# Kernel optimization log

Hardware: AMD Instinct MI355X
Metric: run time of the kernel (lower is better)

Reference implementation:

```python
import jax, jax.numpy as jnp
import numpy as np

N_FILTERS = 1024
KH, KW = 5, 5
LOC = 3                      # locality (pad + maxpool kernel/stride)
B, H, W = 1024, 64, 64
WIN = KH + 2 * LOC           # 11: sliced window side after padding


def setup_inputs() -> dict:
    key = jax.random.key(0)
    k1, k2, k3, k4 = jax.random.split(key, 4)
    X = jax.random.normal(k1, (B, 1, H, W), dtype=jnp.float32)
    weight = jax.random.normal(k2, (N_FILTERS, 1, KH, KW), dtype=jnp.float32)
    bias = jax.random.normal(k3, (N_FILTERS,), dtype=jnp.float32)
    # top-left corner (i, j) of each filter's window in the padded image;
    # must satisfy i + KH + 2*LOC <= H + 2*LOC  =>  i in [0, H-KH]
    positions = jax.random.randint(k4, (N_FILTERS, 2), 0, H - KH + 1, dtype=jnp.int32)
    return {"X": X, "weight": weight, "bias": bias, "positions": positions}


def reference(X, weight, bias, positions):
    # ZeroPad2d(locality)
    Xp = jnp.pad(X, ((0, 0), (0, 0), (LOC, LOC), (LOC, LOC)))

    def slice_one(pos):
        return jax.lax.dynamic_slice(Xp, (0, 0, pos[0], pos[1]), (B, 1, WIN, WIN))

    windows = jax.vmap(slice_one)(positions)
    lhs = jnp.transpose(windows[:, :, 0], (1, 0, 2, 3))

    # All n_filters tiny single-channel convs as ONE grouped conv.
    conv = jax.lax.conv_general_dilated(
        lhs, weight, window_strides=(1, 1), padding='VALID',
        dimension_numbers=('NCHW', 'OIHW', 'NCHW'),
        feature_group_count=N_FILTERS)                # [B,F,2L+1,2L+1] = [B,F,7,7]
    conv = conv + bias[None, :, None, None]

    # MaxPool2d((LOC,LOC)) with default stride=LOC, floor mode -> 2x2.
    pooled = jax.lax.reduce_window(
        conv, -jnp.inf, jax.lax.max,
        window_dimensions=(1, 1, LOC, LOC),
        window_strides=(1, 1, LOC, LOC),
        padding='VALID')                              # [B,F,2,2]

    # torch.cat(dim=1) over per-filter [B,1,2,2] tensors + reshape(B,-1)
    return pooled.reshape(B, -1)                      # [B, F*4]
```

## Files before the change

kernel.cpp:

```cpp
#include <hip/hip_runtime.h>

#define N_FILTERS 1024
#define B_TOTAL   1024
#define IMG       64
#define LDS_ROWS  70
#define LDS_STRIDE 76

__global__ void prep_wt_kernel(const float* __restrict__ W, float* __restrict__ Wt) {
    int idx = blockIdx.x * 256 + threadIdx.x;
    if (idx < 25 * N_FILTERS) {
        int k = idx >> 10;
        int f = idx & (N_FILTERS - 1);
        Wt[idx] = W[f * 25 + k];
    }
}

__global__ __launch_bounds__(256, 4) void filters_main(
    const float* __restrict__ X,
    const float* __restrict__ Wg,
    const float* __restrict__ Wt,
    const float* __restrict__ bias,
    const int*   __restrict__ pos,
    float*       __restrict__ out,
    int use_wt)
{
    __shared__ float L[LDS_ROWS * LDS_STRIDE];
    const int b = blockIdx.x;
    const int t = threadIdx.x;

    for (int idx = t; idx < LDS_ROWS * LDS_STRIDE; idx += 256) L[idx] = 0.0f;
    __syncthreads();

    const float4* X4 = (const float4*)(X + (size_t)b * (IMG * IMG));
    for (int q = t; q < (IMG * IMG / 4); q += 256) {
        int r  = q >> 4;
        int c4 = q & 15;
        float4 v = X4[q];
        *(float4*)&L[(r + 3) * LDS_STRIDE + 4 + (c4 << 2)] = v;
    }
    __syncthreads();

    #pragma unroll 1
    for (int chunk = 0; chunk < 4; ++chunk) {
        const int f = t + (chunk << 8);
        const int i = pos[2 * f];
        const int j = pos[2 * f + 1];

        float w[25];
        if (use_wt) {
            #pragma unroll
            for (int k = 0; k < 25; ++k) w[k] = Wt[k * N_FILTERS + f];
        } else {
            #pragma unroll
            for (int k = 0; k < 25; ++k) w[k] = Wg[f * 25 + k];
        }

        float acc[6][6];
        #pragma unroll
        for (int y = 0; y < 6; ++y)
            #pragma unroll
            for (int x = 0; x < 6; ++x) acc[y][x] = 0.0f;

        const float* Lb = &L[i * LDS_STRIDE + j + 1];
        #pragma unroll
        for (int wr = 0; wr < 10; ++wr) {
            float in[10];
            #pragma unroll
            for (int wc = 0; wc < 10; ++wc) in[wc] = Lb[wr * LDS_STRIDE + wc];
            #pragma unroll
            for (int y = 0; y < 6; ++y) {
                if (y >= ((wr > 4) ? (wr - 4) : 0) && y <= ((wr < 5) ? wr : 5)) {
                    const int r = wr - y;
                    #pragma unroll
                    for (int x = 0; x < 6; ++x) {
                        #pragma unroll
                        for (int c = 0; c < 5; ++c)
                            acc[y][x] = fmaf(w[r * 5 + c], in[x + c], acc[y][x]);
                    }
                }
            }
        }

        const float bv = bias[f];
        float p[2][2];
        #pragma unroll
        for (int py = 0; py < 2; ++py) {
            #pragma unroll
            for (int px = 0; px < 2; ++px) {
                float m = acc[3 * py][3 * px];
                #pragma unroll
                for (int dy = 0; dy < 3; ++dy)
                    #pragma unroll
                    for (int dx = 0; dx < 3; ++dx)
                        m = fmaxf(m, acc[3 * py + dy][3 * px + dx]);
                p[py][px] = m + bv;
            }
        }

        float4 o;
        o.x = p[0][0]; o.y = p[0][1]; o.z = p[1][0]; o.w = p[1][1];
        *(float4*)&out[(size_t)b * (N_FILTERS * 4) + (f << 2)] = o;
    }
}

extern "C" void kernel_launch(void* const* d_in, const int* in_sizes, int n_in,
                              void* d_out, int out_size, void* d_ws, size_t ws_size,
                              hipStream_t stream) {
    const float* X    = (const float*)d_in[0];
    const float* W    = (const float*)d_in[1];
    const float* bias = (const float*)d_in[2];
    const int*   pos  = (const int*)d_in[3];
    float* out = (float*)d_out;
    float* Wt  = (float*)d_ws;

    const int use_wt = (ws_size >= (size_t)(25 * N_FILTERS * sizeof(float))) ? 1 : 0;
    if (use_wt) {
        prep_wt_kernel<<<(25 * N_FILTERS + 255) / 256, 256, 0, stream>>>(W, Wt);
    }
    filters_main<<<B_TOTAL, 256, 0, stream>>>(X, W, Wt, bias, pos, out, use_wt);
}
```

Baseline: 107.0 us.

## Recast per-filter local convs as fp16 MFMA GEMMs over batch with Toeplitz weights

The image is converted to fp16 and stored in a batch-interleaved octet layout. Each filter's 5x5 kernel is expanded into a Toeplitz-style A matrix (36 outputs by 240 window taps), so the per-filter conv over the batch runs as 16x16x32 MFMA ops instead of scalar FMAs. Work is redistributed to one block per filter and batch quarter. Max-pooling is done through LDS. Precision drops to fp16 inputs, and the fixed-size workspace is assumed large enough without any check.

```diff
diff --git a/kernel.cpp b/kernel.cpp
--- a/kernel.cpp
+++ b/kernel.cpp
@@ -1,105 +1,163 @@
 #include <hip/hip_runtime.h>
 
-#define N_FILTERS 1024
-#define B_TOTAL   1024
-#define IMG       64
-#define LDS_ROWS  70
-#define LDS_STRIDE 76
 
-__global__ void prep_wt_kernel(const float* __restrict__ W, float* __restrict__ Wt) {
-    int idx = blockIdx.x * 256 + threadIdx.x;
-    if (idx < 25 * N_FILTERS) {
-        int k = idx >> 10;
-        int f = idx & (N_FILTERS - 1);
-        Wt[idx] = W[f * 25 + k];
+#define PAD_DIM   70
+#define OCT_BYTES 16384
+#define XH_BYTES  ((size_t)700 * OCT_BYTES)
+#define WF_FILTER 24576
+
+typedef _Float16 v8h __attribute__((ext_vector_type(8)));
+typedef float    v4f __attribute__((ext_vector_type(4)));
+
+__global__ __launch_bounds__(256) void prep_kernel(
+    const float* __restrict__ X, const float* __restrict__ W,
+    const int* __restrict__ pos,
+    _Float16* __restrict__ Xh, _Float16* __restrict__ Wf)
+{
+    const int bid = blockIdx.x;
+    const int t   = threadIdx.x;
+    if (bid < 1024) {
+        __shared__ float T[64 * 65];
+        const int r = bid >> 4, bgrp = bid & 15;
+        #pragma unroll
+        for (int i = 0; i < 16; ++i) {
+            int flat = i * 256 + t;
+            int b = flat >> 6, c = flat & 63;
+            T[b * 65 + c] = X[(size_t)(bgrp * 64 + b) * 4096 + r * 64 + c];
+        }
+        __syncthreads();
+        for (int idx = t; idx < 9 * 64; idx += 256) {
+            int o = idx >> 6, b = idx & 63;
+            v8h v;
+            #pragma unroll
+            for (int e = 0; e < 8; ++e) {
+                int c = 8 * o + e - 3;
+                v[e] = (c >= 0 && c < 64) ? (_Float16)T[b * 65 + c] : (_Float16)0.f;
+            }
+            *(v8h*)((char*)Xh + (size_t)((r + 3) * 10 + o) * OCT_BYTES
+                              + (bgrp * 64 + b) * 16) = v;
+        }
+    } else if (bid < 1148) {
+        int zi = bid - 1024, oct;
+        if (zi < 60) { int pr = zi / 10; pr = pr < 3 ? pr : pr + 64; oct = pr * 10 + zi % 10; }
+        else         { oct = (3 + (zi - 60)) * 10 + 9; }
+        uint4* q = (uint4*)((char*)Xh + (size_t)oct * OCT_BYTES);
+        uint4 z = {0, 0, 0, 0};
+        for (int i = t; i < 1024; i += 256) q[i] = z;
+    } else {
+        const int f = bid - 1148;
+        __shared__ _Float16 wl[25];
+        if (t < 25) wl[t] = (_Float16)W[f * 25 + t];
+        const int sjoff = pos[2 * f + 1] & 7;
+        __syncthreads();
+        for (int flat = t; flat < 1536; flat += 256) {
+            int s  = flat / 192;
+            int r1 = flat - s * 192;
+            int mt = r1 >> 6, ln = r1 & 63;
+            int m    = mt * 16 + (ln & 15);
+            int kb   = s * 32 + (ln >> 4) * 8;
+            v8h v;
+            if (m < 36 && kb < 240) {
+                int y  = (m * 43) >> 8;
+                int x  = m - 6 * y;
+                int wr = (kb * 171) >> 12;
+                int r_ = wr - y;
+                int rem0 = kb - wr * 24;
+                #pragma unroll
+                for (int e = 0; e < 8; ++e) {
+                    int c_ = (rem0 + e - sjoff) - x;
+                    bool ok = (r_ >= 0 && r_ < 5 && c_ >= 0 && c_ < 5);
+                    int wi = ok ? (r_ * 5 + c_) : 0;
+                    _Float16 wv = wl[wi];
+                    v[e] = ok ? wv : (_Float16)0.f;
+                }
+            } else {
+                #pragma unroll
+                for (int e = 0; e < 8; ++e) v[e] = (_Float16)0.f;
+            }
+            *(v8h*)((char*)Wf + (size_t)f * WF_FILTER + flat * 16) = v;
+        }
     }
 }
 
 __global__ __launch_bounds__(256, 4) void filters_main(
-    const float* __restrict__ X,
-    const float* __restrict__ Wg,
-    const float* __restrict__ Wt,
-    const float* __restrict__ bias,
-    const int*   __restrict__ pos,
-    float*       __restrict__ out,
-    int use_wt)
+    const _Float16* __restrict__ Xh, const _Float16* __restrict__ Wf,
+    const float* __restrict__ bias, const int* __restrict__ pos,
+    float* __restrict__ out)
 {
-    __shared__ float L[LDS_ROWS * LDS_STRIDE];
-    const int b = blockIdx.x;
-    const int t = threadIdx.x;
+    __shared__ float PL[4][16 * 48];
+    __shared__ float PQ[4][64];
 
-    for (int idx = t; idx < LDS_ROWS * LDS_STRIDE; idx += 256) L[idx] = 0.0f;
-    __syncthreads();
+    const int t    = threadIdx.x;
+    const int lane = t & 63;
+    const int wv   = t >> 6;
+    const int bg   = blockIdx.x & 3;
+    const int f    = blockIdx.x >> 2;
 
-    const float4* X4 = (const float4*)(X + (size_t)b * (IMG * IMG));
-    for (int q = t; q < (IMG * IMG / 4); q += 256) {
-        int r  = q >> 4;
-        int c4 = q & 15;
-        float4 v = X4[q];
-        *(float4*)&L[(r + 3) * LDS_STRIDE + 4 + (c4 << 2)] = v;
+    const int si = pos[2 * f], sj = pos[2 * f + 1];
+    const int o0 = sj >> 3;
+    const int n16 = lane & 15, quad = lane >> 4;
+
+    v4f acc[3][4];
+    #pragma unroll
+    for (int mt = 0; mt < 3; ++mt)
+        #pragma unroll
+        for (int i = 0; i < 4; ++i) acc[mt][i] = (v4f)0.0f;
+
+    const char* xb = (const char*)Xh + (size_t)(bg * 256 + wv * 64 + n16) * 16;
+    const char* wb = (const char*)Wf + (size_t)f * WF_FILTER + lane * 16;
+
+    #pragma unroll
+    for (int s = 0; s < 8; ++s) {
+        int kb  = s * 32 + quad * 8;
+        int wr  = (kb * 171) >> 12;
+        int sub = (kb - wr * 24) >> 3;
+        int oct = (si + wr) * 10 + o0 + sub;
+        oct = (kb < 240) ? oct : 0;
+        const char* bp = xb + (size_t)oct * OCT_BYTES;
+        v8h B0 = *(const v8h*)(bp);
+        v8h B1 = *(const v8h*)(bp + 256);
+        v8h B2 = *(const v8h*)(bp + 512);
+        v8h B3 = *(const v8h*)(bp + 768);
+        const char* ap = wb + s * 3072;
+        v8h A0 = *(const v8h*)(ap);
+        v8h A1 = *(const v8h*)(ap + 1024);
+        v8h A2 = *(const v8h*)(ap + 2048);
+        acc[0][0] = __builtin_amdgcn_mfma_f32_16x16x32_f16(A0, B0, acc[0][0], 0, 0, 0);
+        acc[0][1] = __builtin_amdgcn_mfma_f32_16x16x32_f16(A0, B1, acc[0][1], 0, 0, 0);
+        acc[0][2] = __builtin_amdgcn_mfma_f32_16x16x32_f16(A0, B2, acc[0][2], 0, 0, 0);
+        acc[0][3] = __builtin_amdgcn_mfma_f32_16x16x32_f16(A0, B3, acc[0][3], 0, 0, 0);
+        acc[1][0] = __builtin_amdgcn_mfma_f32_16x16x32_f16(A1, B0, acc[1][0], 0, 0, 0);
+        acc[1][1] = __builtin_amdgcn_mfma_f32_16x16x32_f16(A1, B1, acc[1][1], 0, 0, 0);
+        acc[1][2] = __builtin_amdgcn_mfma_f32_16x16x32_f16(A1, B2, acc[1][2], 0, 0, 0);
+        acc[1][3] = __builtin_amdgcn_mfma_f32_16x16x32_f16(A1, B3, acc[1][3], 0, 0, 0);
+        acc[2][0] = __builtin_amdgcn_mfma_f32_16x16x32_f16(A2, B0, acc[2][0], 0, 0, 0);
+        acc[2][1] = __builtin_amdgcn_mfma_f32_16x16x32_f16(A2, B1, acc[2][1], 0, 0, 0);
+        acc[2][2] = __builtin_amdgcn_mfma_f32_16x16x32_f16(A2, B2, acc[2][2], 0, 0, 0);
+        acc[2][3] = __builtin_amdgcn_mfma_f32_16x16x32_f16(A2, B3, acc[2][3], 0, 0, 0);
     }
-    __syncthreads();
 
-    #pragma unroll 1
-    for (int chunk = 0; chunk < 4; ++chunk) {
-        const int f = t + (chunk << 8);
-        const int i = pos[2 * f];
-        const int j = pos[2 * f + 1];
-
-        float w[25];
-        if (use_wt) {
+    float* pl = PL[wv];
+    float* pq = PQ[wv];
+    const float bv = bias[f];
+    const int py = quad >> 1, px = quad & 1;
+    #pragma unroll
+    for (int i = 0; i < 4; ++i) {
+        #pragma unroll
+        for (int mt = 0; mt < 3; ++mt)
+            *(v4f*)&pl[n16 * 48 + mt * 16 + quad * 4] = acc[mt][i];
+        float mx = pl[n16 * 48 + (3 * py) * 6 + 3 * px];
+        #pragma unroll
+        for (int y = 0; y < 3; ++y)
             #pragma unroll
-            for (int k = 0; k < 25; ++k) w[k] = Wt[k * N_FILTERS + f];
-        } else {
-            #pragma unroll
-            for (int k = 0; k < 25; ++k) w[k] = Wg[f * 25 + k];
+            for (int x = 0; x < 3; ++x)
+                mx = fmaxf(mx, pl[n16 * 48 + (3 * py + y) * 6 + (3 * px + x)]);
+        pq[n16 * 4 + quad] = mx + bv;
+        if (lane < 16) {
+            v4f o = *(v4f*)&pq[lane * 4];
+            int b = bg * 256 + (wv * 4 + i) * 16 + lane;
+            *(v4f*)&out[(size_t)b * 4096 + f * 4] = o;
         }
-
-        float acc[6][6];
-        #pragma unroll
-        for (int y = 0; y < 6; ++y)
-            #pragma unroll
-            for (int x = 0; x < 6; ++x) acc[y][x] = 0.0f;
-
-        const float* Lb = &L[i * LDS_STRIDE + j + 1];
-        #pragma unroll
-        for (int wr = 0; wr < 10; ++wr) {
-            float in[10];
-            #pragma unroll
-            for (int wc = 0; wc < 10; ++wc) in[wc] = Lb[wr * LDS_STRIDE + wc];
-            #pragma unroll
-            for (int y = 0; y < 6; ++y) {
-                if (y >= ((wr > 4) ? (wr - 4) : 0) && y <= ((wr < 5) ? wr : 5)) {
-                    const int r = wr - y;
-                    #pragma unroll
-                    for (int x = 0; x < 6; ++x) {
-                        #pragma unroll
-                        for (int c = 0; c < 5; ++c)
-                            acc[y][x] = fmaf(w[r * 5 + c], in[x + c], acc[y][x]);
-                    }
-                }
-            }
-        }
-
-        const float bv = bias[f];
-        float p[2][2];
-        #pragma unroll
-        for (int py = 0; py < 2; ++py) {
-            #pragma unroll
-            for (int px = 0; px < 2; ++px) {
-                float m = acc[3 * py][3 * px];
-                #pragma unroll
-                for (int dy = 0; dy < 3; ++dy)
-                    #pragma unroll
-                    for (int dx = 0; dx < 3; ++dx)
-                        m = fmaxf(m, acc[3 * py + dy][3 * px + dx]);
-                p[py][px] = m + bv;
-            }
-        }
-
-        float4 o;
-        o.x = p[0][0]; o.y = p[0][1]; o.z = p[1][0]; o.w = p[1][1];
-        *(float4*)&out[(size_t)b * (N_FILTERS * 4) + (f << 2)] = o;
     }
 }
 
@@ -111,11 +169,9 @@
     const float* bias = (const float*)d_in[2];
     const int*   pos  = (const int*)d_in[3];
     float* out = (float*)d_out;
-    float* Wt  = (float*)d_ws;
+    _Float16* Xh = (_Float16*)d_ws;
+    _Float16* Wf = (_Float16*)((char*)d_ws + XH_BYTES);
 
-    const int use_wt = (ws_size >= (size_t)(25 * N_FILTERS * sizeof(float))) ? 1 : 0;
-    if (use_wt) {
-        prep_wt_kernel<<<(25 * N_FILTERS + 255) / 256, 256, 0, stream>>>(W, Wt);
-    }
-    filters_main<<<B_TOTAL, 256, 0, stream>>>(X, W, Wt, bias, pos, out, use_wt);
+    prep_kernel<<<2172, 256, 0, stream>>>(X, W, pos, Xh, Wf);
+    filters_main<<<4096, 256, 0, stream>>>(Xh, Wf, bias, pos, out);
 }
```

Measured after the change: 124.1 us. 1.16x slower.
